# Performance work log

Hardware: AMD Instinct MI355X
Metric: run time of the kernel (lower is better)

Reference implementation:

```python
import jax, jax.numpy as jnp
import numpy as np

HEADS = 8
DIM_HEAD = 64
SCALE = DIM_HEAD ** -0.5


def setup_inputs() -> dict:
    key = jax.random.key(0)
    k1, k2, k3 = jax.random.split(key, 3)
    b, dim, n = 4, 256, 2048
    hidden = HEADS * DIM_HEAD  # 512
    x = jax.random.normal(k1, (b, dim, n), dtype=jnp.float32)
    # Conv1d kernel-size-1 weights are pointwise linear maps over channels.
    w_qkv = jax.random.normal(k2, (3 * hidden, dim), dtype=jnp.float32) * (dim ** -0.5)
    w_out = jax.random.normal(k3, (dim, hidden), dtype=jnp.float32) * (hidden ** -0.5)
    b_out = jnp.zeros((dim,), dtype=jnp.float32)
    return {"x": x, "w_qkv": w_qkv, "w_out": w_out, "b_out": b_out}


def reference(x, w_qkv, w_out, b_out):
    b, dim, n = x.shape
    hidden = w_out.shape[1]
    # pointwise conv1d == channel matmul: [3h, dim] x [b, dim, n] -> [b, 3h, n]
    qkv = jnp.einsum('oi,bin->bon', w_qkv, x)
    q, k, v = jnp.split(qkv, 3, axis=1)
    # b (h c) n -> b h c n
    reshape = lambda t: t.reshape(b, HEADS, DIM_HEAD, n)
    q, k, v = reshape(q) * SCALE, reshape(k), reshape(v)
    sim = jnp.einsum('bhdi,bhdj->bhij', q, k)          # [b, h, n, n]
    attn = jax.nn.softmax(sim, axis=-1)
    out = jnp.einsum('bhij,bhdj->bhid', attn, v)        # [b, h, n, d]
    # b h n d -> b (h d) n
    out = out.transpose(0, 1, 3, 2).reshape(b, hidden, n)
    return jnp.einsum('oi,bin->bon', w_out, out) + b_out[None, :, None]
```

## Files before the change

### kernel.cpp

```cpp
#include <hip/hip_runtime.h>
#include <stdint.h>

#define SEQ  2048
#define DIMC 256
#define HID  512
#define NH   8
#define DH   64

typedef __attribute__((ext_vector_type(8))) short bf16x8;
typedef __attribute__((ext_vector_type(4))) float f32x4;
typedef __attribute__((ext_vector_type(16))) float f32x16;
typedef __attribute__((ext_vector_type(2))) unsigned uint2v;
typedef __attribute__((address_space(1))) const uint32_t guint_t;
typedef __attribute__((address_space(3))) uint32_t luint_t;

__device__ __forceinline__ void gld16(const void* g, void* l) {
  __builtin_amdgcn_global_load_lds((guint_t*)g, (luint_t*)l, 16, 0, 0);
}

__device__ __forceinline__ void barrier_raw() {
  asm volatile("" ::: "memory");
  __builtin_amdgcn_s_barrier();
  asm volatile("" ::: "memory");
}
#define WAITVM(n) asm volatile("s_waitcnt vmcnt(" #n ")" ::: "memory")

__device__ __forceinline__ unsigned short f2bf(float f) {
  union { float f; uint32_t u; } v; v.f = f;
  return (unsigned short)((v.u + 0x7FFFu + ((v.u >> 16) & 1u)) >> 16);
}

__device__ __forceinline__ uint32_t fbits(float f) {
  union { float f; uint32_t u; } v; v.f = f; return v.u;
}

__device__ __forceinline__ uint32_t pku(uint32_t u0, uint32_t u1) {
  return __builtin_amdgcn_perm(u1 + 0x8000u, u0 + 0x8000u, 0x07060302u);
}

__device__ __forceinline__ void swap32(uint32_t& a, uint32_t& b) {
#if __has_builtin(__builtin_amdgcn_permlane32_swap)
  uint2v r = __builtin_amdgcn_permlane32_swap(a, b, false, false);
  a = r[0]; b = r[1];
#else
  uint32_t aw = __shfl_xor(a, 32);
  uint32_t bw = __shfl_xor(b, 32);
  bool lo = (threadIdx.x & 32) == 0;
  uint32_t an = lo ? a : bw;
  uint32_t bn = lo ? aw : b;
  a = an; b = bn;
#endif
}

__global__ __launch_bounds__(256) void prep_kernel(
    const float* __restrict__ x, const float* __restrict__ wqkv,
    const float* __restrict__ wout,
    unsigned short* __restrict__ wqkv_b, unsigned short* __restrict__ wout_b,
    unsigned short* __restrict__ xT) {
  __shared__ float tile[64][65];
  int blk = blockIdx.x;
  int t = threadIdx.x;
  if (blk < 384) {
    int idx = blk * 1024 + t * 4;
    float4 v = *(const float4*)(wqkv + idx);
    float s = ((idx >> 8) < HID) ? 0.18033688011112042f : 1.0f;
    ushort4 o;
    o.x = f2bf(v.x * s); o.y = f2bf(v.y * s);
    o.z = f2bf(v.z * s); o.w = f2bf(v.w * s);
    *(ushort4*)(wqkv_b + idx) = o;
    return;
  }
  if (blk < 512) {
    int idx = (blk - 384) * 1024 + t * 4;
    float4 v = *(const float4*)(wout + idx);
    ushort4 o;
    o.x = f2bf(v.x); o.y = f2bf(v.y); o.z = f2bf(v.z); o.w = f2bf(v.w);
    *(ushort4*)(wout_b + idx) = o;
    return;
  }
  int tid = blk - 512;
  int b  = tid >> 7;
  int r  = tid & 127;
  int i0 = (r >> 5) * 64;
  int n0 = (r & 31) * 64;
  const float* xb = x + (size_t)b * DIMC * SEQ;
  int tn = t & 15, ti = t >> 4;
#pragma unroll
  for (int j = 0; j < 4; j++) {
    int il = ti + j * 16;
    float4 v = *(const float4*)(xb + (size_t)(i0 + il) * SEQ + n0 + tn * 4);
    tile[il][tn*4+0] = v.x; tile[il][tn*4+1] = v.y;
    tile[il][tn*4+2] = v.z; tile[il][tn*4+3] = v.w;
  }
  __syncthreads();
  unsigned short* xTb = xT + (size_t)b * SEQ * DIMC;
#pragma unroll
  for (int j = 0; j < 4; j++) {
    int nl = ti + j * 16;
    int i4 = tn * 4;
    uint2 pk;
    pk.x = (uint32_t)f2bf(tile[i4+0][nl]) | ((uint32_t)f2bf(tile[i4+1][nl]) << 16);
    pk.y = (uint32_t)f2bf(tile[i4+2][nl]) | ((uint32_t)f2bf(tile[i4+3][nl]) << 16);
    *(uint2*)(xTb + (size_t)(n0 + nl) * DIMC + i0 + i4) = pk;
  }
}

__global__ __launch_bounds__(256, 2) void qkv_gemm(
    const unsigned short* __restrict__ wq, const unsigned short* __restrict__ xT,
    unsigned short* __restrict__ Qs, unsigned short* __restrict__ Ks,
    unsigned short* __restrict__ Vt) {
  __shared__ unsigned short lds[32768];
  int o0 = blockIdx.x * 128;
  int n0 = blockIdx.y * 128;
  int b  = blockIdx.z;
  int t  = threadIdx.x;
  int wv = t >> 6, l = t & 63, l15 = l & 15, q = l >> 4;
  int wm = (wv & 1) * 64, wn = (wv >> 1) * 64;
  f32x4 acc[4][4];
#pragma unroll
  for (int i = 0; i < 4; i++)
#pragma unroll
    for (int j = 0; j < 4; j++) acc[i][j] = (f32x4){0.f, 0.f, 0.f, 0.f};
  const unsigned short* Ag = wq + (size_t)o0 * DIMC;
  const unsigned short* Bg = xT + ((size_t)b * SEQ + n0) * DIMC;
  int lrow8 = l >> 3, lcol = l & 7;

  auto stage = [&](int kk, int buf) {
    unsigned short* la = lds + (buf << 14);
    unsigned short* lb = la + 8192;
    int k0 = kk * 64;
#pragma unroll
    for (int c0 = 0; c0 < 4; c0++) {
      int c = wv * 4 + c0;
      int row = c * 8 + lrow8;
      int sg = lcol ^ (row & 7);
      gld16(Ag + (size_t)row * DIMC + k0 + sg * 8, la + c * 512);
      gld16(Bg + (size_t)row * DIMC + k0 + sg * 8, lb + c * 512);
    }
  };

  stage(0, 0);
  for (int kk = 0; kk < 4; kk++) {
    int cur = kk & 1;
    if (kk < 3) { stage(kk + 1, cur ^ 1); WAITVM(8); }
    else        { WAITVM(0); }
    barrier_raw();
    unsigned short* la = lds + (cur << 14);
    unsigned short* lb = la + 8192;
#pragma unroll
    for (int kh = 0; kh < 2; kh++) {
      bf16x8 af[4], bfr[4];
#pragma unroll
      for (int mt = 0; mt < 4; mt++) {
        int row = wm + mt*16 + l15;
        af[mt] = *(const bf16x8*)(la + row*64 + ((kh*4 + q) ^ (row & 7)) * 8);
      }
#pragma unroll
      for (int nt = 0; nt < 4; nt++) {
        int row = wn + nt*16 + l15;
        bfr[nt] = *(const bf16x8*)(lb + row*64 + ((kh*4 + q) ^ (row & 7)) * 8);
      }
#pragma unroll
      for (int mt = 0; mt < 4; mt++)
#pragma unroll
        for (int nt = 0; nt < 4; nt++)
          acc[mt][nt] = __builtin_amdgcn_mfma_f32_16x16x32_bf16(af[mt], bfr[nt], acc[mt][nt], 0, 0, 0);
    }
    barrier_raw();
  }
  int seg3 = o0 >> 9;
  int h0   = (o0 & 511) >> 6;
  if (seg3 == 2) {
#pragma unroll
    for (int mt = 0; mt < 4; mt++)
#pragma unroll
      for (int nt = 0; nt < 4; nt++)
#pragma unroll
        for (int r = 0; r < 4; r++) {
          int ol = wm + mt * 16 + q * 4 + r;
          int h = h0 + (ol >> 6), d = ol & 63;
          int n = n0 + wn + nt * 16 + l15;
          Vt[(((size_t)b * NH + h) * DH + d) * SEQ + n] = f2bf(acc[mt][nt][r]);
        }
  } else {
    unsigned short* dst = (seg3 == 0) ? Qs : Ks;
#pragma unroll
    for (int mt = 0; mt < 4; mt++)
#pragma unroll
      for (int nt = 0; nt < 4; nt++)
#pragma unroll
        for (int r = 0; r < 4; r++) {
          int ol = wm + mt * 16 + q * 4 + r;
          int nn = wn + nt * 16 + l15;
          lds[nn * 136 + ol] = f2bf(acc[mt][nt][r]);
        }
    __syncthreads();
#pragma unroll
    for (int i = 0; i < 8; i++) {
      int idx = i * 256 + t;
      int nn  = idx >> 4;
      int olb = (idx & 15) * 8;
      uint4 v = *(const uint4*)(lds + nn * 136 + olb);
      int h = h0 + (olb >> 6), d = olb & 63;
      *(uint4*)(dst + (((size_t)b * NH + h) * SEQ + n0 + nn) * DH + d) = v;
    }
  }
}

__global__ __launch_bounds__(256, 2) void attn_kernel(
    const unsigned short* __restrict__ Qs, const unsigned short* __restrict__ Ks,
    const unsigned short* __restrict__ Vt, unsigned short* __restrict__ AO) {
  __shared__ unsigned short KVs[32768];
  __shared__ float Lc[256];
  int n0 = blockIdx.x * 128;
  int bh = blockIdx.y;
  int b = bh >> 3, h = bh & 7;
  int t = threadIdx.x;
  int w = t >> 6, l = t & 63, l31 = l & 31, lh = l >> 5, l7 = l & 7;
  int cg = w >> 1, qg = w & 1;
  const unsigned short* Qg = Qs + ((size_t)bh * SEQ + n0 + qg * 64) * DH;
  bf16x8 qb[2][4];
#pragma unroll
  for (int qt = 0; qt < 2; qt++)
#pragma unroll
    for (int kc = 0; kc < 4; kc++)
      qb[qt][kc] = *(const bf16x8*)(Qg + (qt*32 + l31) * DH + kc*16 + lh*8);
  f32x16 oacc[2][2];
  float lrowp[2] = {0.f, 0.f};
#pragma unroll
  for (int qt = 0; qt < 2; qt++)
#pragma unroll
    for (int dt = 0; dt < 2; dt++)
#pragma unroll
      for (int r = 0; r < 16; r++) oacc[qt][dt][r] = 0.f;

  auto stage = [&](int it2, int buf) {
    int jb = it2 * 64;
    unsigned short* base = KVs + (buf << 14);
    if (w < 2) {
      const unsigned short* src = Ks + ((size_t)bh * SEQ + w * 1024 + jb) * DH;
      unsigned short* dst = base + w * 4096;
#pragma unroll
      for (int g = 0; g < 8; g++) {
        int kr = g * 8 + (l >> 3);
        gld16(src + (size_t)kr * DH + (l7 ^ (kr & 7)) * 8, dst + g * 512);
      }
    } else {
      const unsigned short* src = Vt + (size_t)bh * DH * SEQ + (w - 2) * 1024 + jb;
      unsigned short* dst = base + 8192 + (w - 2) * 4096;
#pragma unroll
      for (int g = 0; g < 8; g++) {
        int dr = g * 8 + (l >> 3);
        gld16(src + (size_t)dr * SEQ + (l7 ^ (dr & 7)) * 8, dst + g * 512);
      }
    }
  };

  stage(0, 0);
  for (int it = 0; it < 16; it++) {
    int cur = it & 1;
    if (it < 15) { stage(it + 1, cur ^ 1); WAITVM(8); }
    else         { WAITVM(0); }
    barrier_raw();
    const unsigned short* Kst = KVs + (cur << 14) + cg * 4096;
    const unsigned short* Vst = KVs + (cur << 14) + 8192 + cg * 4096;
#pragma unroll
    for (int kb = 0; kb < 64; kb += 32) {
      f32x16 st[2];
#pragma unroll
      for (int qt = 0; qt < 2; qt++)
#pragma unroll
        for (int r = 0; r < 16; r++) st[qt][r] = 0.f;
#pragma unroll
      for (int kc = 0; kc < 4; kc++) {
        bf16x8 kf = *(const bf16x8*)(Kst + (kb + l31) * 64 + (((kc*2 + lh) ^ l7)) * 8);
        st[0] = __builtin_amdgcn_mfma_f32_32x32x16_bf16(kf, qb[0][kc], st[0], 0, 0, 0);
        st[1] = __builtin_amdgcn_mfma_f32_32x32x16_bf16(kf, qb[1][kc], st[1], 0, 0, 0);
      }
      bf16x8 vf[2][2];
#pragma unroll
      for (int kc2 = 0; kc2 < 2; kc2++)
#pragma unroll
        for (int dt = 0; dt < 2; dt++)
          vf[kc2][dt] = *(const bf16x8*)(Vst + (dt*32 + l31) * 64 +
                                         ((((kb >> 3) + kc2*2 + lh) ^ l7)) * 8);
#pragma unroll
      for (int qt = 0; qt < 2; qt++) {
        float p[16];
        float s0 = 0.f;
#pragma unroll
        for (int r = 0; r < 16; r++) { p[r] = __builtin_amdgcn_exp2f(st[qt][r]); s0 += p[r]; }
        lrowp[qt] += s0;
        bf16x8 af[2];
#pragma unroll
        for (int hf = 0; hf < 2; hf++) {
          uint32_t xs[4], ys[4];
#pragma unroll
          for (int j = 0; j < 4; j++) {
            xs[j] = fbits(p[hf*8 + j]);
            ys[j] = fbits(p[hf*8 + 4 + j]);
            swap32(xs[j], ys[j]);
          }
          uint32_t d0 = pku(xs[0], xs[1]);
          uint32_t d1 = pku(xs[2], xs[3]);
          uint32_t d2 = pku(ys[0], ys[1]);
          uint32_t d3 = pku(ys[2], ys[3]);
          union { uint32_t u[4]; bf16x8 v; } cv;
          cv.u[0] = d0; cv.u[1] = d1; cv.u[2] = d2; cv.u[3] = d3;
          af[hf] = cv.v;
        }
#pragma unroll
        for (int kc2 = 0; kc2 < 2; kc2++)
#pragma unroll
          for (int dt = 0; dt < 2; dt++)
            oacc[qt][dt] = __builtin_amdgcn_mfma_f32_32x32x16_bf16(af[kc2], vf[kc2][dt], oacc[qt][dt], 0, 0, 0);
      }
    }
    barrier_raw();
  }
#pragma unroll
  for (int qt = 0; qt < 2; qt++) {
    float v = lrowp[qt];
    v += __shfl_xor(v, 32);
    if (l < 32) Lc[cg * 128 + qg * 64 + qt * 32 + l31] = v;
  }
  __syncthreads();
  float* Oc = (float*)KVs;
  if (cg == 1) {
#pragma unroll
    for (int qt = 0; qt < 2; qt++)
#pragma unroll
      for (int dt = 0; dt < 2; dt++)
#pragma unroll
        for (int r = 0; r < 16; r++) {
          int qrow = qg*64 + qt*32 + (r & 3) + 8*(r >> 2) + 4*lh;
          Oc[qrow * 64 + dt*32 + l31] = oacc[qt][dt][r];
        }
  }
  __syncthreads();
  if (cg == 0) {
    unsigned short* AOb = AO + (size_t)b * SEQ * HID + h * DH;
#pragma unroll
    for (int qt = 0; qt < 2; qt++)
#pragma unroll
      for (int r = 0; r < 16; r++) {
        int qrow = qg*64 + qt*32 + (r & 3) + 8*(r >> 2) + 4*lh;
        float inv = __builtin_amdgcn_rcpf(Lc[qrow] + Lc[128 + qrow]);
        int n = n0 + qrow;
#pragma unroll
        for (int dt = 0; dt < 2; dt++) {
          float val = (oacc[qt][dt][r] + Oc[qrow * 64 + dt*32 + l31]) * inv;
          AOb[(size_t)n * HID + dt*32 + l31] = f2bf(val);
        }
      }
  }
}

__global__ __launch_bounds__(256, 2) void out_gemm(
    const unsigned short* __restrict__ wo, const unsigned short* __restrict__ AO,
    const float* __restrict__ bias, float* __restrict__ out) {
  __shared__ unsigned short lds[24576];
  int o0 = blockIdx.x * 64;
  int n0 = blockIdx.y * 128;
  int b  = blockIdx.z;
  int t  = threadIdx.x;
  int wv = t >> 6, l = t & 63, l15 = l & 15, q = l >> 4;
  int wm = (wv & 1) * 32, wn = (wv >> 1) * 64;
  f32x4 acc[2][4];
#pragma unroll
  for (int i = 0; i < 2; i++)
#pragma unroll
    for (int j = 0; j < 4; j++) acc[i][j] = (f32x4){0.f,0.f,0.f,0.f};
  const unsigned short* Ag = wo + (size_t)o0 * HID;
  const unsigned short* Bg = AO + ((size_t)b * SEQ + n0) * HID;
  int lrow8 = l >> 3, lcol = l & 7;

  auto stage = [&](int kk, int buf) {
    unsigned short* la = lds + buf * 12288;
    unsigned short* lb = la + 4096;
    int k0 = kk * 64;
#pragma unroll
    for (int c0 = 0; c0 < 2; c0++) {
      int c = wv * 2 + c0;
      int row = c * 8 + lrow8;
      int sg = lcol ^ (row & 7);
      gld16(Ag + (size_t)row * HID + k0 + sg * 8, la + c * 512);
    }
#pragma unroll
    for (int c0 = 0; c0 < 4; c0++) {
      int c = wv * 4 + c0;
      int row = c * 8 + lrow8;
      int sg = lcol ^ (row & 7);
      gld16(Bg + (size_t)row * HID + k0 + sg * 8, lb + c * 512);
    }
  };

  stage(0, 0);
  for (int kk = 0; kk < 8; kk++) {
    int cur = kk & 1;
    if (kk < 7) { stage(kk + 1, cur ^ 1); WAITVM(6); }
    else        { WAITVM(0); }
    barrier_raw();
    unsigned short* la = lds + cur * 12288;
    unsigned short* lb = la + 4096;
#pragma unroll
    for (int kh = 0; kh < 2; kh++) {
      bf16x8 af[2], bfr[4];
#pragma unroll
      for (int mt = 0; mt < 2; mt++) {
        int row = wm + mt*16 + l15;
        af[mt] = *(const bf16x8*)(la + row*64 + ((kh*4 + q) ^ (row & 7)) * 8);
      }
#pragma unroll
      for (int nt = 0; nt < 4; nt++) {
        int row = wn + nt*16 + l15;
        bfr[nt] = *(const bf16x8*)(lb + row*64 + ((kh*4 + q) ^ (row & 7)) * 8);
      }
#pragma unroll
      for (int mt = 0; mt < 2; mt++)
#pragma unroll
        for (int nt = 0; nt < 4; nt++)
          acc[mt][nt] = __builtin_amdgcn_mfma_f32_16x16x32_bf16(af[mt], bfr[nt], acc[mt][nt], 0,0,0);
    }
    barrier_raw();
  }
#pragma unroll
  for (int mt = 0; mt < 2; mt++)
#pragma unroll
    for (int nt = 0; nt < 4; nt++)
#pragma unroll
      for (int r = 0; r < 4; r++) {
        int o2 = o0 + wm + mt*16 + q*4 + r;
        int n  = n0 + wn + nt*16 + l15;
        out[((size_t)b * DIMC + o2) * SEQ + n] = acc[mt][nt][r] + bias[o2];
      }
}

extern "C" void kernel_launch(void* const* d_in, const int* in_sizes, int n_in,
                              void* d_out, int out_size, void* d_ws, size_t ws_size,
                              hipStream_t stream) {
  const float* x    = (const float*)d_in[0];
  const float* wqkv = (const float*)d_in[1];
  const float* wout = (const float*)d_in[2];
  const float* bout = (const float*)d_in[3];
  float* out = (float*)d_out;
  char* ws = (char*)d_ws;
  unsigned short* wqkv_b = (unsigned short*)(ws);
  unsigned short* wout_b = (unsigned short*)(ws + 786432);
  unsigned short* xT     = (unsigned short*)(ws + 1048576);
  unsigned short* Qs     = (unsigned short*)(ws + 5242880);
  unsigned short* Ks     = (unsigned short*)(ws + 13631488);
  unsigned short* Vt     = (unsigned short*)(ws + 22020096);
  unsigned short* AO     = (unsigned short*)(ws + 30408704);
  prep_kernel<<<1024, 256, 0, stream>>>(x, wqkv, wout, wqkv_b, wout_b, xT);
  qkv_gemm<<<dim3(12, 16, 4), 256, 0, stream>>>(wqkv_b, xT, Qs, Ks, Vt);
  attn_kernel<<<dim3(16, 32), 256, 0, stream>>>(Qs, Ks, Vt, AO);
  out_gemm<<<dim3(4, 16, 4), 256, 0, stream>>>(wout_b, AO, bout, out);
}
```

Baseline: 129.4 us.

## Shrink attention tiles to 64 queries per block and remap grid for occupancy

Each attention block now handles 64 query rows instead of 128, with each wave owning 32 queries and half the keys. K/V staging shrinks to 32-key chunks with a reswizzled V layout, which halves LDS use and raises launch bounds to 4 blocks per SM. The grid becomes 1024 one-dimensional blocks with a block-to-(batch,head) mapping that interleaves heads, so concurrent blocks spread across heads for better cache locality. K/V is reloaded twice as often per query and there are more barrier iterations per block.

```diff
diff --git a/kernel.cpp b/kernel.cpp
--- a/kernel.cpp
+++ b/kernel.cpp
@@ -207,152 +207,139 @@
   }
 }
 
-__global__ __launch_bounds__(256, 2) void attn_kernel(
+__global__ __launch_bounds__(256, 4) void attn_kernel(
     const unsigned short* __restrict__ Qs, const unsigned short* __restrict__ Ks,
     const unsigned short* __restrict__ Vt, unsigned short* __restrict__ AO) {
-  __shared__ unsigned short KVs[32768];
-  __shared__ float Lc[256];
-  int n0 = blockIdx.x * 128;
-  int bh = blockIdx.y;
+  __shared__ unsigned short KVs[16384];
+  __shared__ float Lc[128];
+  int id = blockIdx.x;
+  int s  = id >> 3;
+  int bh = (id & 7) * 4 + (s & 3);
+  int q0 = (s >> 2) * 64;
   int b = bh >> 3, h = bh & 7;
   int t = threadIdx.x;
-  int w = t >> 6, l = t & 63, l31 = l & 31, lh = l >> 5, l7 = l & 7;
-  int cg = w >> 1, qg = w & 1;
-  const unsigned short* Qg = Qs + ((size_t)bh * SEQ + n0 + qg * 64) * DH;
-  bf16x8 qb[2][4];
-#pragma unroll
-  for (int qt = 0; qt < 2; qt++)
-#pragma unroll
-    for (int kc = 0; kc < 4; kc++)
-      qb[qt][kc] = *(const bf16x8*)(Qg + (qt*32 + l31) * DH + kc*16 + lh*8);
-  f32x16 oacc[2][2];
-  float lrowp[2] = {0.f, 0.f};
-#pragma unroll
-  for (int qt = 0; qt < 2; qt++)
-#pragma unroll
-    for (int dt = 0; dt < 2; dt++)
-#pragma unroll
-      for (int r = 0; r < 16; r++) oacc[qt][dt][r] = 0.f;
+  int w = t >> 6, l = t & 63, l31 = l & 31, lh = l >> 5;
+  int cg = w & 1, qg = w >> 1;
+  const unsigned short* Qg = Qs + ((size_t)bh * SEQ + q0 + qg * 32) * DH;
+  bf16x8 qb[4];
+#pragma unroll
+  for (int kc = 0; kc < 4; kc++)
+    qb[kc] = *(const bf16x8*)(Qg + l31 * DH + kc*16 + lh*8);
+  f32x16 oacc[2];
+  float lsum = 0.f;
+#pragma unroll
+  for (int dt = 0; dt < 2; dt++)
+#pragma unroll
+    for (int r = 0; r < 16; r++) oacc[dt][r] = 0.f;
+
+  const unsigned short* Ksrc = Ks + ((size_t)bh * SEQ + cg * 1024) * DH;
+  const unsigned short* Vsrc = Vt + (size_t)bh * DH * SEQ + cg * 1024;
 
   auto stage = [&](int it2, int buf) {
-    int jb = it2 * 64;
-    unsigned short* base = KVs + (buf << 14);
+    int jb = it2 * 32;
+    unsigned short* base = KVs + buf * 8192;
     if (w < 2) {
-      const unsigned short* src = Ks + ((size_t)bh * SEQ + w * 1024 + jb) * DH;
-      unsigned short* dst = base + w * 4096;
-#pragma unroll
-      for (int g = 0; g < 8; g++) {
+      const unsigned short* src = Ksrc + (size_t)jb * DH;
+      unsigned short* dst = base + cg * 2048;
+#pragma unroll
+      for (int g = 0; g < 4; g++) {
         int kr = g * 8 + (l >> 3);
-        gld16(src + (size_t)kr * DH + (l7 ^ (kr & 7)) * 8, dst + g * 512);
+        gld16(src + (size_t)kr * DH + ((l & 7) ^ (kr & 7)) * 8, dst + g * 512);
       }
     } else {
-      const unsigned short* src = Vt + (size_t)bh * DH * SEQ + (w - 2) * 1024 + jb;
-      unsigned short* dst = base + 8192 + (w - 2) * 4096;
-#pragma unroll
-      for (int g = 0; g < 8; g++) {
-        int dr = g * 8 + (l >> 3);
-        gld16(src + (size_t)dr * SEQ + (l7 ^ (dr & 7)) * 8, dst + g * 512);
+      const unsigned short* src = Vsrc + jb;
+      unsigned short* dst = base + 4096 + cg * 2048;
+#pragma unroll
+      for (int g = 0; g < 4; g++) {
+        int dr = g * 16 + (l >> 2);
+        gld16(src + (size_t)dr * SEQ + ((l & 3) ^ (dr & 3)) * 8, dst + g * 512);
       }
     }
   };
 
   stage(0, 0);
-  for (int it = 0; it < 16; it++) {
+  for (int it = 0; it < 32; it++) {
     int cur = it & 1;
-    if (it < 15) { stage(it + 1, cur ^ 1); WAITVM(8); }
+    if (it < 31) { stage(it + 1, cur ^ 1); WAITVM(4); }
     else         { WAITVM(0); }
     barrier_raw();
-    const unsigned short* Kst = KVs + (cur << 14) + cg * 4096;
-    const unsigned short* Vst = KVs + (cur << 14) + 8192 + cg * 4096;
-#pragma unroll
-    for (int kb = 0; kb < 64; kb += 32) {
-      f32x16 st[2];
-#pragma unroll
-      for (int qt = 0; qt < 2; qt++)
-#pragma unroll
-        for (int r = 0; r < 16; r++) st[qt][r] = 0.f;
-#pragma unroll
-      for (int kc = 0; kc < 4; kc++) {
-        bf16x8 kf = *(const bf16x8*)(Kst + (kb + l31) * 64 + (((kc*2 + lh) ^ l7)) * 8);
-        st[0] = __builtin_amdgcn_mfma_f32_32x32x16_bf16(kf, qb[0][kc], st[0], 0, 0, 0);
-        st[1] = __builtin_amdgcn_mfma_f32_32x32x16_bf16(kf, qb[1][kc], st[1], 0, 0, 0);
-      }
-      bf16x8 vf[2][2];
-#pragma unroll
-      for (int kc2 = 0; kc2 < 2; kc2++)
-#pragma unroll
-        for (int dt = 0; dt < 2; dt++)
-          vf[kc2][dt] = *(const bf16x8*)(Vst + (dt*32 + l31) * 64 +
-                                         ((((kb >> 3) + kc2*2 + lh) ^ l7)) * 8);
-#pragma unroll
-      for (int qt = 0; qt < 2; qt++) {
-        float p[16];
-        float s0 = 0.f;
-#pragma unroll
-        for (int r = 0; r < 16; r++) { p[r] = __builtin_amdgcn_exp2f(st[qt][r]); s0 += p[r]; }
-        lrowp[qt] += s0;
-        bf16x8 af[2];
-#pragma unroll
-        for (int hf = 0; hf < 2; hf++) {
-          uint32_t xs[4], ys[4];
-#pragma unroll
-          for (int j = 0; j < 4; j++) {
-            xs[j] = fbits(p[hf*8 + j]);
-            ys[j] = fbits(p[hf*8 + 4 + j]);
-            swap32(xs[j], ys[j]);
-          }
-          uint32_t d0 = pku(xs[0], xs[1]);
-          uint32_t d1 = pku(xs[2], xs[3]);
-          uint32_t d2 = pku(ys[0], ys[1]);
-          uint32_t d3 = pku(ys[2], ys[3]);
-          union { uint32_t u[4]; bf16x8 v; } cv;
-          cv.u[0] = d0; cv.u[1] = d1; cv.u[2] = d2; cv.u[3] = d3;
-          af[hf] = cv.v;
-        }
-#pragma unroll
-        for (int kc2 = 0; kc2 < 2; kc2++)
-#pragma unroll
-          for (int dt = 0; dt < 2; dt++)
-            oacc[qt][dt] = __builtin_amdgcn_mfma_f32_32x32x16_bf16(af[kc2], vf[kc2][dt], oacc[qt][dt], 0, 0, 0);
-      }
-    }
-    barrier_raw();
-  }
-#pragma unroll
-  for (int qt = 0; qt < 2; qt++) {
-    float v = lrowp[qt];
+    const unsigned short* Kst = KVs + cur * 8192 + cg * 2048;
+    const unsigned short* Vst = KVs + cur * 8192 + 4096 + cg * 2048;
+    f32x16 st;
+#pragma unroll
+    for (int r = 0; r < 16; r++) st[r] = 0.f;
+#pragma unroll
+    for (int kc = 0; kc < 4; kc++) {
+      bf16x8 kf = *(const bf16x8*)(Kst + l31 * 64 + (((kc*2 + lh)) ^ (l31 & 7)) * 8);
+      st = __builtin_amdgcn_mfma_f32_32x32x16_bf16(kf, qb[kc], st, 0, 0, 0);
+    }
+    bf16x8 vf[2][2];
+#pragma unroll
+    for (int kc2 = 0; kc2 < 2; kc2++)
+#pragma unroll
+      for (int dt = 0; dt < 2; dt++)
+        vf[kc2][dt] = *(const bf16x8*)(Vst + (dt*32 + l31) * 32 +
+                                       (((kc2*2 + lh)) ^ (l31 & 3)) * 8);
+    float p[16];
+    float s0 = 0.f;
+#pragma unroll
+    for (int r = 0; r < 16; r++) { p[r] = __builtin_amdgcn_exp2f(st[r]); s0 += p[r]; }
+    lsum += s0;
+    bf16x8 af[2];
+#pragma unroll
+    for (int hf = 0; hf < 2; hf++) {
+      uint32_t xs[4], ys[4];
+#pragma unroll
+      for (int j = 0; j < 4; j++) {
+        xs[j] = fbits(p[hf*8 + j]);
+        ys[j] = fbits(p[hf*8 + 4 + j]);
+        swap32(xs[j], ys[j]);
+      }
+      uint32_t d0 = pku(xs[0], xs[1]);
+      uint32_t d1 = pku(xs[2], xs[3]);
+      uint32_t d2 = pku(ys[0], ys[1]);
+      uint32_t d3 = pku(ys[2], ys[3]);
+      union { uint32_t u[4]; bf16x8 v; } cv;
+      cv.u[0] = d0; cv.u[1] = d1; cv.u[2] = d2; cv.u[3] = d3;
+      af[hf] = cv.v;
+    }
+#pragma unroll
+    for (int kc2 = 0; kc2 < 2; kc2++)
+#pragma unroll
+      for (int dt = 0; dt < 2; dt++)
+        oacc[dt] = __builtin_amdgcn_mfma_f32_32x32x16_bf16(af[kc2], vf[kc2][dt], oacc[dt], 0, 0, 0);
+    barrier_raw();
+  }
+  {
+    float v = lsum;
     v += __shfl_xor(v, 32);
-    if (l < 32) Lc[cg * 128 + qg * 64 + qt * 32 + l31] = v;
+    if (l < 32) Lc[cg * 64 + qg * 32 + l31] = v;
   }
   __syncthreads();
   float* Oc = (float*)KVs;
   if (cg == 1) {
 #pragma unroll
-    for (int qt = 0; qt < 2; qt++)
-#pragma unroll
-      for (int dt = 0; dt < 2; dt++)
-#pragma unroll
-        for (int r = 0; r < 16; r++) {
-          int qrow = qg*64 + qt*32 + (r & 3) + 8*(r >> 2) + 4*lh;
-          Oc[qrow * 64 + dt*32 + l31] = oacc[qt][dt][r];
-        }
+    for (int dt = 0; dt < 2; dt++)
+#pragma unroll
+      for (int r = 0; r < 16; r++) {
+        int qrow = qg*32 + (r & 3) + 8*(r >> 2) + 4*lh;
+        Oc[qrow * 64 + dt*32 + l31] = oacc[dt][r];
+      }
   }
   __syncthreads();
   if (cg == 0) {
     unsigned short* AOb = AO + (size_t)b * SEQ * HID + h * DH;
 #pragma unroll
-    for (int qt = 0; qt < 2; qt++)
-#pragma unroll
-      for (int r = 0; r < 16; r++) {
-        int qrow = qg*64 + qt*32 + (r & 3) + 8*(r >> 2) + 4*lh;
-        float inv = __builtin_amdgcn_rcpf(Lc[qrow] + Lc[128 + qrow]);
-        int n = n0 + qrow;
-#pragma unroll
-        for (int dt = 0; dt < 2; dt++) {
-          float val = (oacc[qt][dt][r] + Oc[qrow * 64 + dt*32 + l31]) * inv;
-          AOb[(size_t)n * HID + dt*32 + l31] = f2bf(val);
-        }
-      }
+    for (int r = 0; r < 16; r++) {
+      int qrow = qg*32 + (r & 3) + 8*(r >> 2) + 4*lh;
+      float inv = __builtin_amdgcn_rcpf(Lc[qrow] + Lc[64 + qrow]);
+      int n = q0 + qrow;
+#pragma unroll
+      for (int dt = 0; dt < 2; dt++) {
+        float val = (oacc[dt][r] + Oc[qrow * 64 + dt*32 + l31]) * inv;
+        AOb[(size_t)n * HID + dt*32 + l31] = f2bf(val);
+      }
+    }
   }
 }
 
@@ -454,6 +441,6 @@
   unsigned short* AO     = (unsigned short*)(ws + 30408704);
   prep_kernel<<<1024, 256, 0, stream>>>(x, wqkv, wout, wqkv_b, wout_b, xT);
   qkv_gemm<<<dim3(12, 16, 4), 256, 0, stream>>>(wqkv_b, xT, Qs, Ks, Vt);
-  attn_kernel<<<dim3(16, 32), 256, 0, stream>>>(Qs, Ks, Vt, AO);
+  attn_kernel<<<1024, 256, 0, stream>>>(Qs, Ks, Vt, AO);
   out_gemm<<<dim3(4, 16, 4), 256, 0, stream>>>(wout_b, AO, bout, out);
 }
```

Measured after the change: 139.5 us. +7.8%, slower.
